# Optimization experiments

Measured on AMD Instinct MI355X. Metric: run time of the kernel, lower is better.

The kernel has to match this reference:

```python
import jax, jax.numpy as jnp
import numpy as np

# ---- static config ----
B, N, C, HF, WF = 2, 256, 256, 64, 64
PATCH = 512
ROI = 15
MARGIN = (ROI - 1) // 2
HID = 256
HEADS = 8
DEPTH = 3
FFN = 1024
NQ = 16
LN_EPS = 1e-5


def setup_inputs() -> dict:
    key = jax.random.key(0)
    ks = jax.random.split(key, 16)
    p = lambda i, shape: (0.02 * jax.random.normal(ks[i], shape, jnp.float32))
    inp = {
        "image_embeddings": jax.random.normal(ks[0], (B, C, HF, WF), jnp.float32),
        "keypoints": jax.random.uniform(ks[1], (B, N, 2), jnp.float32, 0.0, float(PATCH)),
        "keypoints_valid_mask": jax.random.randint(ks[2], (B, N), 0, 2) == 1,
        "proj_w": p(3, (HID, C)), "proj_b": jnp.zeros((HID,), jnp.float32),
        "query_embed": p(4, (NQ, HID)),
        "self_qkv_w": p(5, (DEPTH, 3 * HID, HID)), "self_qkv_b": jnp.zeros((DEPTH, 3 * HID), jnp.float32),
        "self_out_w": p(6, (DEPTH, HID, HID)), "self_out_b": jnp.zeros((DEPTH, HID), jnp.float32),
        "cross_qkv_w": p(7, (DEPTH, 3 * HID, HID)), "cross_qkv_b": jnp.zeros((DEPTH, 3 * HID), jnp.float32),
        "cross_out_w": p(8, (DEPTH, HID, HID)), "cross_out_b": jnp.zeros((DEPTH, HID), jnp.float32),
        "ffn1_w": p(9, (DEPTH, FFN, HID)), "ffn1_b": jnp.zeros((DEPTH, FFN), jnp.float32),
        "ffn2_w": p(10, (DEPTH, HID, FFN)), "ffn2_b": jnp.zeros((DEPTH, HID), jnp.float32),
        "ln1_w": jnp.ones((DEPTH, HID), jnp.float32), "ln1_b": jnp.zeros((DEPTH, HID), jnp.float32),
        "ln2_w": jnp.ones((DEPTH, HID), jnp.float32), "ln2_b": jnp.zeros((DEPTH, HID), jnp.float32),
        "ln3_w": jnp.ones((DEPTH, HID), jnp.float32), "ln3_b": jnp.zeros((DEPTH, HID), jnp.float32),
        "out_w": p(11, (4, HID)), "out_b": jnp.zeros((4,), jnp.float32),
    }
    return inp


def _layer_norm(x, w, b):
    mu = x.mean(-1, keepdims=True)
    var = ((x - mu) ** 2).mean(-1, keepdims=True)
    return (x - mu) * jax.lax.rsqrt(var + LN_EPS) * w + b


def _mha(q_in, kv_in, Wqkv, bqkv, Wo, bo, pad=None):
    # PyTorch nn.MultiheadAttention math (batch_first). pad: [B, S_kv] True=masked.
    Dh = HID // HEADS
    Wq, Wk, Wv = jnp.split(Wqkv, 3, axis=0)
    bq, bk, bv = jnp.split(bqkv, 3, axis=0)
    Bsz = q_in.shape[0]
    q = (q_in @ Wq.T + bq).reshape(Bsz, -1, HEADS, Dh)
    k = (kv_in @ Wk.T + bk).reshape(Bsz, -1, HEADS, Dh)
    v = (kv_in @ Wv.T + bv).reshape(Bsz, -1, HEADS, Dh)
    s = jnp.einsum('bqhd,bkhd->bhqk', q, k) * (Dh ** -0.5)
    if pad is not None:
        s = jnp.where(pad[:, None, None, :], -jnp.inf, s)
    a = jax.nn.softmax(s, axis=-1)
    o = jnp.einsum('bhqk,bkhd->bqhd', a, v).reshape(Bsz, -1, HID)
    return o @ Wo.T + bo


def _roi_sample(img, keypoints):
    # _get_valid_grid + F.grid_sample(bilinear, align_corners=False, zeros padding)
    rc = jnp.round(keypoints)                               # [B,N,2] (r,c), round-half-even like Python round
    off = jnp.arange(-MARGIN, MARGIN + 1, dtype=img.dtype)  # [ROI]
    gy = rc[:, :, 0][..., None, None] + off[:, None]        # [B,N,ROI,ROI] rows
    gx = rc[:, :, 1][..., None, None] + off[None, :]        # [B,N,ROI,ROI] cols
    gxn = gx / (PATCH - 1) * 2.0 - 1.0
    gyn = gy / (PATCH - 1) * 2.0 - 1.0
    invalid = (gxn < -1) | (gyn < -1) | (gxn > 1) | (gyn > 1)  # [B,N,ROI,ROI]
    gxn = jnp.where(invalid, 0.0, gxn)
    gyn = jnp.where(invalid, 0.0, gyn)
    # unnormalize onto the feature map (align_corners=False)
    x = ((gxn + 1.0) * WF - 1.0) * 0.5
    y = ((gyn + 1.0) * HF - 1.0) * 0.5
    x = x.reshape(B, -1)  # [B, P], P = N*ROI*ROI
    y = y.reshape(B, -1)
    x0f = jnp.floor(x); y0f = jnp.floor(y)
    wx = x - x0f; wy = y - y0f
    x0 = x0f.astype(jnp.int32); y0 = y0f.astype(jnp.int32)
    bidx = jnp.arange(B)[:, None]

    def tap(yi, xi, w):
        ok = (yi >= 0) & (yi < HF) & (xi >= 0) & (xi < WF)
        yc = jnp.clip(yi, 0, HF - 1)
        xc = jnp.clip(xi, 0, WF - 1)
        v = img[bidx, :, yc, xc]                 # [B,P,C] gather
        return v * (w * ok)[..., None]

    out = (tap(y0, x0, (1 - wy) * (1 - wx)) + tap(y0, x0 + 1, (1 - wy) * wx)
           + tap(y0 + 1, x0, wy * (1 - wx)) + tap(y0 + 1, x0 + 1, wy * wx))
    feat = out.reshape(B, N, ROI * ROI, C)
    feat = jnp.where(invalid.reshape(B, N, ROI * ROI)[..., None], 0.0, feat)
    return feat  # [B, N, HW, C]


def reference(image_embeddings, keypoints, keypoints_valid_mask, proj_w, proj_b,
              query_embed, self_qkv_w, self_qkv_b, self_out_w, self_out_b,
              cross_qkv_w, cross_qkv_b, cross_out_w, cross_out_b,
              ffn1_w, ffn1_b, ffn2_w, ffn2_b,
              ln1_w, ln1_b, ln2_w, ln2_b, ln3_w, ln3_b, out_w, out_b):
    feat = _roi_sample(image_embeddings, keypoints)                 # [B,N,HW,C]
    mem = jnp.einsum('bnpc,oc->bnpo', feat, proj_w) + proj_b        # 1x1 conv proj
    mem = mem.reshape(B * N, ROI * ROI, HID)
    pad = jnp.broadcast_to(~keypoints_valid_mask.reshape(-1, 1), (B * N, ROI * ROI))
    pad = pad.at[:, 0].set(False)                                    # token 0 always attendable
    tgt = jnp.broadcast_to(query_embed[None], (B * N, NQ, HID))
    for l in range(DEPTH):  # post-norm TransformerDecoderLayer, relu, eval (no dropout)
        sa = _mha(tgt, tgt, self_qkv_w[l], self_qkv_b[l], self_out_w[l], self_out_b[l])
        tgt = _layer_norm(tgt + sa, ln1_w[l], ln1_b[l])
        ca = _mha(tgt, mem, cross_qkv_w[l], cross_qkv_b[l], cross_out_w[l], cross_out_b[l], pad)
        tgt = _layer_norm(tgt + ca, ln2_w[l], ln2_b[l])
        ff = jax.nn.relu(tgt @ ffn1_w[l].T + ffn1_b[l]) @ ffn2_w[l].T + ffn2_b[l]
        tgt = _layer_norm(tgt + ff, ln3_w[l], ln3_b[l])
    out = tgt @ out_w.T + out_b                                      # [B*N, NQ, 4]
    return out.reshape(B, N, NQ, 4)
```

## Files before the change

kernel.cpp:

```cpp
#include <hip/hip_runtime.h>
#include <hip/hip_fp16.h>

#define LB __launch_bounds__(256)

typedef unsigned short u16;
typedef unsigned int   u32;
typedef __attribute__((ext_vector_type(8))) short bf16x8;
typedef __attribute__((ext_vector_type(4))) float f32x4;
typedef __attribute__((ext_vector_type(8))) u16  u16x8;

__device__ __forceinline__ u16 f2b(float f) {
    u32 u = __float_as_uint(f);
    u32 r = (u + 0x7fffu + ((u >> 16) & 1u)) >> 16;
    return (u16)r;
}
__device__ __forceinline__ float b2f(u16 h) {
    return __uint_as_float((u32)h << 16);
}

#define QSCALE 0.17677669529663687f


__global__ void k_prep(const unsigned char* __restrict__ m, int* __restrict__ valid,
                       const float* __restrict__ pb,
                       const float* __restrict__ cqkv_w,
                       const float* __restrict__ cqkv_b,
                       float* __restrict__ ckv)
{
    if (blockIdx.x == 0) {
        __shared__ int flag;
        if (threadIdx.x == 0) flag = 0;
        __syncthreads();
        int loc = 0;
        for (int off = threadIdx.x; off < 512; off += 256)
            if ((off & 3) != 0 && m[off] != 0) loc = 1;
        if (loc) atomicOr(&flag, 1);
        __syncthreads();
        const bool bytelay = (flag != 0);
        for (int s = threadIdx.x; s < 512; s += 256)
            valid[s] = bytelay ? (int)(m[s] != 0) : (int)(((const int*)m)[s] != 0);
    } else {
        const int l = blockIdx.x - 1;
        const float* Wk = cqkv_w + (size_t)l * 196608 + 65536;
        const float* Wv = cqkv_w + (size_t)l * 196608 + 131072;
        const float* kb = cqkv_b + (size_t)l * 768 + 256;
        const float* vb = cqkv_b + (size_t)l * 768 + 512;
        const int o = threadIdx.x;
        float a = 0.f, c = 0.f;
        for (int cc = 0; cc < 256; cc += 4) {
            const float4 p4 = *(const float4*)(pb + cc);
            const float4 k4 = *(const float4*)(Wk + (size_t)o * 256 + cc);
            const float4 v4 = *(const float4*)(Wv + (size_t)o * 256 + cc);
            a += p4.x * k4.x + p4.y * k4.y + p4.z * k4.z + p4.w * k4.w;
            c += p4.x * v4.x + p4.y * v4.y + p4.z * v4.z + p4.w * v4.w;
        }
        ckv[l * 512 + o]       = a + kb[o];
        ckv[l * 512 + 256 + o] = c + vb[o];
    }
}

__global__ LB void k_wconv(const float* __restrict__ s0, const float* __restrict__ s1,
                           const float* __restrict__ s2, const float* __restrict__ s3,
                           const float* __restrict__ s4, const float* __restrict__ s5,
                           const float* __restrict__ s6, u16* __restrict__ dst)
{
    const int e = blockIdx.x * 256 + threadIdx.x;
    if (e >= 3670016) return;
    float v;
    int i = e;
    if (i < 65536) v = s0[i];
    else if ((i -= 65536) < 589824) v = s1[i];
    else if ((i -= 589824) < 196608) v = s2[i];
    else if ((i -= 196608) < 589824) v = s3[i];
    else if ((i -= 589824) < 196608) v = s4[i];
    else if ((i -= 196608) < 786432) v = s5[i];
    else if ((i -= 786432) < 786432) v = s6[i];
    else if ((i -= 786432) < 393216) {
        const int l = i / 131072;
        const int r = (i - l * 131072) >> 8;
        const int c = i & 255;
        v = s3[(size_t)l * 196608 + (size_t)(256 + r) * 256 + c];
    } else {
        i -= 393216;
        v = s0[(i & 255) * 256 + (i >> 8)];
    }
    dst[e] = f2b(v);
}

__global__ LB void k_transpose(const float* __restrict__ img, u16* __restrict__ imgTb)
{
    __shared__ float tile[64][65];
    const int b  = blockIdx.z;
    const int c0 = blockIdx.y * 64;
    const int p0 = blockIdx.x * 64;
    const int t  = threadIdx.x;
    const int tr = t >> 6, tc = t & 63;
#pragma unroll
    for (int p = 0; p < 16; ++p) {
        const int i = p * 4 + tr;
        tile[i][tc] = img[((size_t)(b * 256 + c0 + i)) * 4096 + p0 + tc];
    }
    __syncthreads();
#pragma unroll
    for (int p = 0; p < 16; ++p) {
        const int jj = p * 4 + tr;
        imgTb[((size_t)(b * 4096 + p0 + jj)) * 256 + c0 + tc] = f2b(tile[tc][jj]);
    }
}

template<int BM>
__global__ LB void gemm_mfma(const u16* __restrict__ A, const u16* __restrict__ W,
                             const float* __restrict__ bias,
                             float* __restrict__ Cf, u16* __restrict__ Cb,
                             int M, int N, int K, int relu)
{
    constexpr int BN = 128;
    __shared__ u16 lds[2][(BM + BN) * 64];
    const int t = threadIdx.x;
    const int wid = t >> 6, lane = t & 63;
    const int bm = blockIdx.y * BM, bn = blockIdx.x * BN;
    const int KT = K >> 6;

    auto stage = [&](int buf, int kt) {
        const int k0 = kt * 64;
        const int rr = t >> 3;
        const int u  = t & 7;
#pragma unroll
        for (int q = 0; q < BM / 32; ++q) {
            const int r = q * 32 + rr;
            const u16* src = A + (size_t)(bm + r) * K + k0 + ((u ^ (r & 7)) << 3);
            __builtin_amdgcn_global_load_lds(
                (const __attribute__((address_space(1))) void*)src,
                (__attribute__((address_space(3))) void*)&lds[buf][q * 2048 + wid * 512],
                16, 0, 0);
        }
#pragma unroll
        for (int q = 0; q < 4; ++q) {
            const int r = q * 32 + rr;
            const u16* src = W + (size_t)(bn + r) * K + k0 + ((u ^ (r & 7)) << 3);
            __builtin_amdgcn_global_load_lds(
                (const __attribute__((address_space(1))) void*)src,
                (__attribute__((address_space(3))) void*)&lds[buf][BM * 64 + q * 2048 + wid * 512],
                16, 0, 0);
        }
    };

    const int wr = wid >> 1, wc = wid & 1;
    constexpr int MR = BM / 32;
    f32x4 acc[MR][4];
    const f32x4 z = {0.f, 0.f, 0.f, 0.f};
#pragma unroll
    for (int mi = 0; mi < MR; ++mi)
#pragma unroll
        for (int ni = 0; ni < 4; ++ni) acc[mi][ni] = z;

    const int r16 = lane & 15, kg = lane >> 4;

    stage(0, 0);
    int cur = 0;
    for (int kt = 0; kt < KT; ++kt) {
        asm volatile("s_waitcnt vmcnt(0)" ::: "memory");
        __syncthreads();
        if (kt + 1 < KT) stage(cur ^ 1, kt + 1);
        const u16* pA = lds[cur];
        const u16* pB = lds[cur] + BM * 64;
#pragma unroll
        for (int kk = 0; kk < 2; ++kk) {
            const int s = kk * 4 + kg;
            bf16x8 afr[MR], bfr[4];
#pragma unroll
            for (int mi = 0; mi < MR; ++mi) {
                const int r = wr * (BM / 2) + mi * 16 + r16;
                afr[mi] = *(const bf16x8*)(pA + r * 64 + ((s ^ (r & 7)) << 3));
            }
#pragma unroll
            for (int ni = 0; ni < 4; ++ni) {
                const int c = wc * 64 + ni * 16 + r16;
                bfr[ni] = *(const bf16x8*)(pB + c * 64 + ((s ^ (c & 7)) << 3));
            }
#pragma unroll
            for (int mi = 0; mi < MR; ++mi)
#pragma unroll
                for (int ni = 0; ni < 4; ++ni)
                    acc[mi][ni] = __builtin_amdgcn_mfma_f32_16x16x32_bf16(
                        afr[mi], bfr[ni], acc[mi][ni], 0, 0, 0);
        }
        cur ^= 1;
    }

#pragma unroll
    for (int mi = 0; mi < MR; ++mi) {
#pragma unroll
        for (int ni = 0; ni < 4; ++ni) {
            const int col = bn + wc * 64 + ni * 16 + r16;
            const float bs = bias ? bias[col] : 0.0f;
#pragma unroll
            for (int rg = 0; rg < 4; ++rg) {
                const int row = bm + wr * (BM / 2) + mi * 16 + kg * 4 + rg;
                float v = acc[mi][ni][rg] + bs;
                if (relu) v = fmaxf(v, 0.0f);
                if (Cf) Cf[(size_t)row * N + col] = v;
                if (Cb) Cb[(size_t)row * N + col] = f2b(v);
            }
        }
    }
}

__global__ LB void gemm_ln(const u16* __restrict__ A, const u16* __restrict__ W,
                           const float* __restrict__ bias,
                           float* __restrict__ tgt, u16* __restrict__ tgtb,
                           const float* __restrict__ lnw, const float* __restrict__ lnb,
                           int K,
                           const float* __restrict__ ow, const float* __restrict__ ob,
                           float* __restrict__ outp)
{
    __shared__ u16 lA[32 * 64];
    __shared__ u16 lB[256 * 64];
    __shared__ float psum[2][32];
    __shared__ float psq[2][32];
    __shared__ float hsum[2][32][4];
    const int t = threadIdx.x;
    const int wid = t >> 6, lane = t & 63;
    const int r16 = lane & 15, kg = lane >> 4;
    const int wr = wid >> 1, wc = wid & 1;
    const int bm = blockIdx.x * 32;
    const int KT = K >> 6;

    f32x4 acc[8];
    const f32x4 z = {0.f, 0.f, 0.f, 0.f};
#pragma unroll
    for (int ni = 0; ni < 8; ++ni) acc[ni] = z;

    for (int kt = 0; kt < KT; ++kt) {
        const int k0 = kt * 64;
        const int rr = t >> 3;
        const int u  = t & 7;
        {
            const int r = rr;
            const u16* src = A + (size_t)(bm + r) * K + k0 + ((u ^ (r & 7)) << 3);
            __builtin_amdgcn_global_load_lds(
                (const __attribute__((address_space(1))) void*)src,
                (__attribute__((address_space(3))) void*)&lA[wid * 512],
                16, 0, 0);
        }
#pragma unroll
        for (int q = 0; q < 8; ++q) {
            const int r = q * 32 + rr;
            const u16* src = W + (size_t)r * K + k0 + ((u ^ (r & 7)) << 3);
            __builtin_amdgcn_global_load_lds(
                (const __attribute__((address_space(1))) void*)src,
                (__attribute__((address_space(3))) void*)&lB[q * 2048 + wid * 512],
                16, 0, 0);
        }
        asm volatile("s_waitcnt vmcnt(0)" ::: "memory");
        __syncthreads();
#pragma unroll
        for (int kk = 0; kk < 2; ++kk) {
            const int s = kk * 4 + kg;
            const int ra = wr * 16 + r16;
            const bf16x8 afr = *(const bf16x8*)(lA + ra * 64 + ((s ^ (ra & 7)) << 3));
#pragma unroll
            for (int ni = 0; ni < 8; ++ni) {
                const int c = wc * 128 + ni * 16 + r16;
                const bf16x8 bfr = *(const bf16x8*)(lB + c * 64 + ((s ^ (c & 7)) << 3));
                acc[ni] = __builtin_amdgcn_mfma_f32_16x16x32_bf16(afr, bfr, acc[ni], 0, 0, 0);
            }
        }
        __syncthreads();
    }

    float xv[4][8];
    float bcol[8], wcol[8], bncol[8];
#pragma unroll
    for (int ni = 0; ni < 8; ++ni) {
        const int c = wc * 128 + ni * 16 + r16;
        bcol[ni]  = bias[c];
        wcol[ni]  = lnw[c];
        bncol[ni] = lnb[c];
    }
#pragma unroll
    for (int rg = 0; rg < 4; ++rg) {
        const int row = bm + wr * 16 + kg * 4 + rg;
#pragma unroll
        for (int ni = 0; ni < 8; ++ni) {
            const int c = wc * 128 + ni * 16 + r16;
            xv[rg][ni] = tgt[(size_t)row * 256 + c] + acc[ni][rg] + bcol[ni];
        }
    }
#pragma unroll
    for (int rg = 0; rg < 4; ++rg) {
        float s = 0.f;
#pragma unroll
        for (int ni = 0; ni < 8; ++ni) s += xv[rg][ni];
#pragma unroll
        for (int m = 1; m < 16; m <<= 1) s += __shfl_xor(s, m);
        if (r16 == 0) psum[wc][wr * 16 + kg * 4 + rg] = s;
    }
    __syncthreads();
    float mu[4];
#pragma unroll
    for (int rg = 0; rg < 4; ++rg) {
        const int rl = wr * 16 + kg * 4 + rg;
        mu[rg] = (psum[0][rl] + psum[1][rl]) * (1.0f / 256.0f);
    }
#pragma unroll
    for (int rg = 0; rg < 4; ++rg) {
        float q = 0.f;
#pragma unroll
        for (int ni = 0; ni < 8; ++ni) {
            const float d = xv[rg][ni] - mu[rg];
            q += d * d;
        }
#pragma unroll
        for (int m = 1; m < 16; m <<= 1) q += __shfl_xor(q, m);
        if (r16 == 0) psq[wc][wr * 16 + kg * 4 + rg] = q;
    }
    __syncthreads();
    float onorm[4][8];
#pragma unroll
    for (int rg = 0; rg < 4; ++rg) {
        const int rl = wr * 16 + kg * 4 + rg;
        const int row = bm + rl;
        const float var = (psq[0][rl] + psq[1][rl]) * (1.0f / 256.0f);
        const float inv = 1.0f / sqrtf(var + 1e-5f);
#pragma unroll
        for (int ni = 0; ni < 8; ++ni) {
            const int c = wc * 128 + ni * 16 + r16;
            const float o = (xv[rg][ni] - mu[rg]) * inv * wcol[ni] + bncol[ni];
            onorm[rg][ni] = o;
            tgt[(size_t)row * 256 + c]  = o;
            tgtb[(size_t)row * 256 + c] = f2b(o);
        }
    }

    if (outp) {
#pragma unroll
        for (int j = 0; j < 4; ++j) {
            float wj[8];
#pragma unroll
            for (int ni = 0; ni < 8; ++ni)
                wj[ni] = ow[j * 256 + wc * 128 + ni * 16 + r16];
#pragma unroll
            for (int rg = 0; rg < 4; ++rg) {
                float p = 0.f;
#pragma unroll
                for (int ni = 0; ni < 8; ++ni) p += onorm[rg][ni] * wj[ni];
#pragma unroll
                for (int m = 1; m < 16; m <<= 1) p += __shfl_xor(p, m);
                if (r16 == 0) hsum[wc][wr * 16 + kg * 4 + rg][j] = p;
            }
        }
        __syncthreads();
        if (t < 128) {
            const int row = t >> 2, j = t & 3;
            outp[(size_t)(bm + row) * 4 + j] =
                hsum[0][row][j] + hsum[1][row][j] + ob[j];
        }
    }
}

__global__ LB void k_init_tgt(float* __restrict__ tgt, u16* __restrict__ tgtb,
                              const float* __restrict__ qe)
{
    const int e = blockIdx.x * 256 + threadIdx.x;
    const int c = e & 255;
    const int row = e >> 8;
    const int i = row & 15;
    const float v = qe[(i << 8) | c];
    tgt[e] = v;
    tgtb[e] = f2b(v);
}

__global__ LB void k_self_attn(const u16* __restrict__ QKV, u16* __restrict__ O)
{
    __shared__ __align__(16) u16 arena[4][1536];
    const int t = threadIdx.x;
    const int lane = t & 63, wid = t >> 6;
    const int r16 = lane & 15, kg = lane >> 4;
    const int blk = blockIdx.x;
    const int s = blk >> 1;
    const int h = (blk & 1) * 4 + wid;

    u16* p_lds = &arena[wid][0];
    u16* vT    = &arena[wid][512];

    const bf16x8 qfr = *(const bf16x8*)(QKV + (size_t)(s * 16 + r16) * 768 + h * 32 + kg * 8);
    const bf16x8 kfr = *(const bf16x8*)(QKV + (size_t)(s * 16 + r16) * 768 + 256 + h * 32 + kg * 8);
    f32x4 sv = {0.f, 0.f, 0.f, 0.f};
    sv = __builtin_amdgcn_mfma_f32_16x16x32_bf16(qfr, kfr, sv, 0, 0, 0);

    float ev[4], rowsum[4];
#pragma unroll
    for (int rg = 0; rg < 4; ++rg) ev[rg] = sv[rg] * QSCALE;
#pragma unroll
    for (int rg = 0; rg < 4; ++rg) {
        float mx = ev[rg];
#pragma unroll
        for (int m = 1; m < 16; m <<= 1) mx = fmaxf(mx, __shfl_xor(mx, m));
        ev[rg] = __expf(ev[rg] - mx);
        float ps = ev[rg];
#pragma unroll
        for (int m = 1; m < 16; m <<= 1) ps += __shfl_xor(ps, m);
        rowsum[rg] = ps;
    }

#pragma unroll
    for (int rg = 0; rg < 4; ++rg)
        p_lds[(kg * 4 + rg) * 32 + r16] = f2b(ev[rg]);
    {
        const int zq = lane & 15, zc = 16 + (lane >> 4) * 4;
#pragma unroll
        for (int j = 0; j < 4; ++j) p_lds[zq * 32 + zc + j] = 0;
    }
    {
        const int key = lane >> 2, ch8 = (lane & 3) * 8;
        const u16x8 v = *(const u16x8*)(QKV + (size_t)(s * 16 + key) * 768 + 512 + h * 32 + ch8);
#pragma unroll
        for (int j = 0; j < 8; ++j)
            vT[(ch8 + j) * 32 + key] = ((const u16*)&v)[j];
        const int zc0 = lane >> 1, zk0 = 16 + (lane & 1) * 8;
#pragma unroll
        for (int j = 0; j < 8; ++j) vT[zc0 * 32 + zk0 + j] = 0;
    }

#pragma unroll
    for (int ct = 0; ct < 2; ++ct) {
        const bf16x8 pa = *(const bf16x8*)(p_lds + r16 * 32 + kg * 8);
        const bf16x8 vb = *(const bf16x8*)(vT + (ct * 16 + r16) * 32 + kg * 8);
        f32x4 ao = {0.f, 0.f, 0.f, 0.f};
        ao = __builtin_amdgcn_mfma_f32_16x16x32_bf16(pa, vb, ao, 0, 0, 0);
#pragma unroll
        for (int rg = 0; rg < 4; ++rg) {
            const int q = kg * 4 + rg;
            O[(size_t)(s * 16 + q) * 256 + h * 32 + ct * 16 + r16] = f2b(ao[rg] / rowsum[rg]);
        }
    }
}

__global__ LB void k_cross_attn(const u16* __restrict__ Qb,
                                const u16* __restrict__ KV, int kvs,
                                const float* __restrict__ ckv,
                                const int* __restrict__ valid,
                                const float* __restrict__ kps,
                                u16* __restrict__ O)
{
    __shared__ __align__(16) char arena[64832];
    u16* Wm  = (u16*)arena;
    u16* WmT = (u16*)(arena + 14400);

    const int t = threadIdx.x;
    const int lane = t & 63, wid = t >> 6;
    const int r16 = lane & 15, kg = lane >> 4;
    const int blk = blockIdx.x;
    const int s = blk >> 1;
    const int h = (blk & 1) * 4 + wid;
    const int b = s >> 8, n = s & 255;

    u16* buf = (u16*)(arena + 22848 + wid * 10496);
    u16* p_b = (u16*)(arena + 22848 + wid * 10496 + 2048);
    u16* QP  = p_b;

    for (int e = t; e < 16208; e += 256) ((u32*)arena)[e] = 0;
    __syncthreads();

    const float kpy = kps[(b * 256 + n) * 2 + 0];
    const float kpx = kps[(b * 256 + n) * 2 + 1];
    const float gx0 = rintf(kpx) - 7.0f;
    const float gy0 = rintf(kpy) - 7.0f;
    const float gxn0 = gx0 / 511.0f * 2.0f - 1.0f;
    const float gyn0 = gy0 / 511.0f * 2.0f - 1.0f;
    const float xb = ((gxn0 + 1.f) * 64.f - 1.f) * 0.5f;
    const float yb = ((gyn0 + 1.f) * 64.f - 1.f) * 0.5f;
    const int x0b = (int)floorf(xb);
    const int y0b = (int)floorf(yb);

    if (t < 225) {
        const int iy = t / 15, ix = t - iy * 15;
        const float gy = rintf(kpy) + (float)(iy - 7);
        const float gx = rintf(kpx) + (float)(ix - 7);
        const float gxn = gx / 511.0f * 2.0f - 1.0f;
        const float gyn = gy / 511.0f * 2.0f - 1.0f;
        const bool inval = (gxn < -1.f) || (gyn < -1.f) || (gxn > 1.f) || (gyn > 1.f);
        const float x = ((gxn + 1.f) * 64.f - 1.f) * 0.5f;
        const float y = ((gyn + 1.f) * 64.f - 1.f) * 0.5f;
        const float x0f = floorf(x), y0f = floorf(y);
        const float wx = x - x0f, wy = y - y0f;
        const int x0 = (int)x0f, y0 = (int)y0f;
#pragma unroll
        for (int tt = 0; tt < 4; ++tt) {
            const int dy = tt >> 1, dx = tt & 1;
            const int yi = y0 + dy, xi = x0 + dx;
            const bool ok = (yi >= 0) && (yi < 64) && (xi >= 0) && (xi < 64) && !inval;
            const float w = (dy ? wy : 1.f - wy) * (dx ? wx : 1.f - wx);
            if (ok) {
                const int cell = (yi - y0b) * 4 + (xi - x0b);
                const u16 wb = f2b(w);
                Wm[t * 32 + ((((cell >> 3) ^ (t & 3)) << 3) | (cell & 7))] = wb;
                WmT[cell * 264 + t] = wb;
            }
        }
    }
    const int cell = lane >> 2, ch8 = (lane & 3) * 8;
    const int cy = cell >> 2, cx = cell & 3;
    const int py = min(max(y0b + cy, 0), 63);
    const int px = min(max(x0b + cx, 0), 63);
    const size_t texidx = (size_t)(b * 4096 + py * 64 + px) * kvs + h * 32 + ch8;
    *(u16x8*)(buf + cell * 32 + ch8) = *(const u16x8*)(KV + texidx);
    const bool vld = valid[s] != 0;
    __syncthreads();

    {
        const bf16x8 qfr = *(const bf16x8*)(Qb + (size_t)(s * 16 + r16) * 256 + h * 32 + kg * 8);
        const bf16x8 tfr = *(const bf16x8*)(buf + r16 * 32 + kg * 8);
        f32x4 aq = {0.f, 0.f, 0.f, 0.f};
        aq = __builtin_amdgcn_mfma_f32_16x16x32_bf16(qfr, tfr, aq, 0, 0, 0);
#pragma unroll
        for (int rg = 0; rg < 4; ++rg)
            QP[(kg * 4 + rg) * 40 + r16] = f2b(aq[rg]);
    }

    float ev[4][15];
    {
        const bf16x8 afr = *(const bf16x8*)(QP + r16 * 40 + kg * 8);
#pragma unroll
        for (int tile = 0; tile < 15; ++tile) {
            const int p = tile * 16 + r16;
            const int rc = p < 225 ? p : 224;
            const bf16x8 bfr = *(const bf16x8*)(Wm + rc * 32 + ((kg ^ (rc & 3)) << 3));
            f32x4 acc = {0.f, 0.f, 0.f, 0.f};
            acc = __builtin_amdgcn_mfma_f32_16x16x32_bf16(afr, bfr, acc, 0, 0, 0);
#pragma unroll
            for (int rg = 0; rg < 4; ++rg) {
                float sv = acc[rg] * QSCALE;
                if (p > 224) sv = -1e30f;
                if (!vld && p > 0) sv = -1e30f;
                ev[rg][tile] = sv;
            }
        }
    }
    float rowsumv[4];
#pragma unroll
    for (int rg = 0; rg < 4; ++rg) {
        float mx = -1e30f;
#pragma unroll
        for (int k = 0; k < 15; ++k) mx = fmaxf(mx, ev[rg][k]);
#pragma unroll
        for (int m = 1; m < 16; m <<= 1) mx = fmaxf(mx, __shfl_xor(mx, m));
        float ps = 0.f;
#pragma unroll
        for (int k = 0; k < 15; ++k) {
            ev[rg][k] = __expf(ev[rg][k] - mx);
            ps += ev[rg][k];
        }
#pragma unroll
        for (int m = 1; m < 16; m <<= 1) ps += __shfl_xor(ps, m);
        rowsumv[rg] = ps;
    }

#pragma unroll
    for (int rg = 0; rg < 4; ++rg)
#pragma unroll
        for (int k = 0; k < 15; ++k) {
            const int p = k * 16 + r16;
            if (p < 225) p_b[(kg * 4 + rg) * 264 + p] = f2b(ev[rg][k]);
        }
    for (int e = lane; e < 496; e += 64) {
        const int row = e / 31;
        p_b[row * 264 + 225 + (e - row * 31)] = 0;
    }

    {
        const u16x8 v = *(const u16x8*)(KV + texidx + 256);
#pragma unroll
        for (int j = 0; j < 8; ++j)
            buf[(ch8 + j) * 32 + cell] = ((const u16*)&v)[j];
        const int zr = lane & 15, zc0 = 16 + (lane >> 4) * 4;
#pragma unroll
        for (int j = 0; j < 4; ++j) buf[zr * 32 + zc0 + j] = 0;
    }

    f32x4 pw = {0.f, 0.f, 0.f, 0.f};
#pragma unroll
    for (int ks = 0; ks < 8; ++ks) {
        const bf16x8 pa = *(const bf16x8*)(p_b + r16 * 264 + ks * 32 + kg * 8);
        const bf16x8 wb = *(const bf16x8*)(WmT + r16 * 264 + ks * 32 + kg * 8);
        pw = __builtin_amdgcn_mfma_f32_16x16x32_bf16(pa, wb, pw, 0, 0, 0);
    }

#pragma unroll
    for (int rg = 0; rg < 4; ++rg)
        QP[(kg * 4 + rg) * 40 + r16] = f2b(pw[rg]);
    {
        const int zq = lane & 15, zc0 = 16 + (lane >> 4) * 4;
#pragma unroll
        for (int j = 0; j < 4; ++j) QP[zq * 40 + zc0 + j] = 0;
    }

#pragma unroll
    for (int ct = 0; ct < 2; ++ct) {
        const bf16x8 pa = *(const bf16x8*)(QP + r16 * 40 + kg * 8);
        const bf16x8 vb = *(const bf16x8*)(buf + (ct * 16 + r16) * 32 + kg * 8);
        f32x4 ao = {0.f, 0.f, 0.f, 0.f};
        ao = __builtin_amdgcn_mfma_f32_16x16x32_bf16(pa, vb, ao, 0, 0, 0);
#pragma unroll
        for (int rg = 0; rg < 4; ++rg) {
            const int q = kg * 4 + rg;
            const int ch = h * 32 + ct * 16 + r16;
            const float val = ao[rg] / rowsumv[rg] + ckv[256 + ch];
            O[(size_t)(s * 16 + q) * 256 + ch] = f2b(val);
        }
    }
}

extern "C" void kernel_launch(void* const* d_in, const int* in_sizes, int n_in,
                              void* d_out, int out_size, void* d_ws, size_t ws_size,
                              hipStream_t stream)
{
    const float* img          = (const float*)d_in[0];
    const float* kps          = (const float*)d_in[1];
    const unsigned char* vmsk = (const unsigned char*)d_in[2];
    const float* proj_w       = (const float*)d_in[3];
    const float* proj_b       = (const float*)d_in[4];
    const float* query_embed  = (const float*)d_in[5];
    const float* self_qkv_w   = (const float*)d_in[6];
    const float* self_qkv_b   = (const float*)d_in[7];
    const float* self_out_w   = (const float*)d_in[8];
    const float* self_out_b   = (const float*)d_in[9];
    const float* cross_qkv_w  = (const float*)d_in[10];
    const float* cross_qkv_b  = (const float*)d_in[11];
    const float* cross_out_w  = (const float*)d_in[12];
    const float* cross_out_b  = (const float*)d_in[13];
    const float* ffn1_w       = (const float*)d_in[14];
    const float* ffn1_b       = (const float*)d_in[15];
    const float* ffn2_w       = (const float*)d_in[16];
    const float* ffn2_b       = (const float*)d_in[17];
    const float* ln1_w        = (const float*)d_in[18];
    const float* ln1_b        = (const float*)d_in[19];
    const float* ln2_w        = (const float*)d_in[20];
    const float* ln2_b        = (const float*)d_in[21];
    const float* ln3_w        = (const float*)d_in[22];
    const float* ln3_b        = (const float*)d_in[23];
    const float* out_w        = (const float*)d_in[24];
    const float* out_b        = (const float*)d_in[25];
    float* out = (float*)d_out;

    char* W8 = (char*)d_ws;
    size_t off = 0;
    auto alloc = [&](size_t bytes) { void* p = W8 + off; off += (bytes + 255) & ~(size_t)255; return p; };
    float* tgt   = (float*)alloc(2097152 * 4);
    u16* Qb      = (u16*)alloc(2097152 * 2);
    u16* Sb16    = (u16*)alloc(6291456 * 2);
    float* ckv   = (float*)alloc(3 * 512 * 4);
    u16* imgTb   = (u16*)alloc(2097152 * 2);
    u16* KVb3    = (u16*)alloc(12582912 * 2);
    u16* tgtb    = (u16*)alloc(2097152 * 2);
    u16* Abuf    = (u16*)alloc(2097152 * 2);
    u16* Hbuf    = (u16*)alloc(8388608 * 2);
    u16* wAll    = (u16*)alloc(3670016 * 2);
    u16* WcombB  = (u16*)alloc(393216 * 2);
    int* valid   = (int*)alloc(512 * 4);

    u16* wProj  = wAll;
    u16* wSQKV  = wProj + 65536;
    u16* wSOut  = wSQKV + 589824;
    u16* wCQKV  = wSOut + 196608;
    u16* wCOut  = wCQKV + 589824;
    u16* wF1    = wCOut + 196608;
    u16* wF2    = wF1 + 786432;
    u16* wCKV3  = wF2 + 786432;
    u16* wProjT = wCKV3 + 393216;

    k_prep<<<4, 256, 0, stream>>>(vmsk, valid, proj_b, cross_qkv_w, cross_qkv_b, ckv);
    k_wconv<<<14336, 256, 0, stream>>>(proj_w, self_qkv_w, self_out_w, cross_qkv_w,
                                       cross_out_w, ffn1_w, ffn2_w, wAll);
    k_transpose<<<dim3(64, 4, 2), 256, 0, stream>>>(img, imgTb);
    gemm_mfma<64><<<dim3(2, 24), 256, 0, stream>>>(wCKV3, wProjT, nullptr,
                                                   nullptr, WcombB, 1536, 256, 256, 0);
    gemm_mfma<128><<<dim3(12, 64), 256, 0, stream>>>(imgTb, WcombB, nullptr,
                                                     nullptr, KVb3, 8192, 1536, 256, 0);
    k_init_tgt<<<8192, 256, 0, stream>>>(tgt, tgtb, query_embed);

    for (int l = 0; l < 3; ++l) {
        const int last = (l == 2);
        gemm_mfma<64><<<dim3(6, 128), 256, 0, stream>>>(tgtb, wSQKV + (size_t)l * 196608,
            self_qkv_b + (size_t)l * 768, nullptr, Sb16, 8192, 768, 256, 0);
        k_self_attn<<<1024, 256, 0, stream>>>(Sb16, Abuf);
        gemm_ln<<<256, 256, 0, stream>>>(Abuf, wSOut + (size_t)l * 65536,
            self_out_b + (size_t)l * 256, tgt, tgtb,
            ln1_w + (size_t)l * 256, ln1_b + (size_t)l * 256, 256,
            nullptr, nullptr, nullptr);

        gemm_mfma<64><<<dim3(2, 128), 256, 0, stream>>>(tgtb, wCQKV + (size_t)l * 196608,
            cross_qkv_b + (size_t)l * 768, nullptr, Qb, 8192, 256, 256, 0);
        k_cross_attn<<<1024, 256, 0, stream>>>(Qb, KVb3 + (size_t)l * 512, 1536,
                                               ckv + (size_t)l * 512, valid, kps, Abuf);
        gemm_ln<<<256, 256, 0, stream>>>(Abuf, wCOut + (size_t)l * 65536,
            cross_out_b + (size_t)l * 256, tgt, tgtb,
            ln2_w + (size_t)l * 256, ln2_b + (size_t)l * 256, 256,
            nullptr, nullptr, nullptr);

        gemm_mfma<64><<<dim3(8, 128), 256, 0, stream>>>(tgtb, wF1 + (size_t)l * 262144,
            ffn1_b + (size_t)l * 1024, nullptr, Hbuf, 8192, 1024, 256, 1);
        gemm_ln<<<256, 256, 0, stream>>>(Hbuf, wF2 + (size_t)l * 262144,
            ffn2_b + (size_t)l * 256, tgt, tgtb,
            ln3_w + (size_t)l * 256, ln3_b + (size_t)l * 256, 1024,
            last ? out_w : nullptr, last ? out_b : nullptr, last ? out : nullptr);
    }
}
```

Baseline: 378.3 us.

## Fuse cross-attention Q projection into attention kernel and merge prep into weight conversion

The per-layer Q projection GEMM for cross-attention is removed; each attention block now computes its head's Q slice from tgtb and the bf16 Q weights with MFMA and stores it into shared memory, adding the Q bias from the ckv buffer. The k_prep kernel is folded into k_wconv as extra blocks. The K-bias precomputation is replaced by storing the raw Q bias, since the K-side constant shifts every score in a row equally and so cancels in softmax. This saves three launches and the Qb round trip through global memory. In exchange each block repeats the tgt row loads, and the two blocks per sample each read 8 K-steps of weights.

```diff
diff --git a/kernel.cpp b/kernel.cpp
--- a/kernel.cpp
+++ b/kernel.cpp
@@ -21,49 +21,45 @@
 #define QSCALE 0.17677669529663687f
 
 
-__global__ void k_prep(const unsigned char* __restrict__ m, int* __restrict__ valid,
-                       const float* __restrict__ pb,
-                       const float* __restrict__ cqkv_w,
-                       const float* __restrict__ cqkv_b,
-                       float* __restrict__ ckv)
-{
-    if (blockIdx.x == 0) {
-        __shared__ int flag;
-        if (threadIdx.x == 0) flag = 0;
-        __syncthreads();
-        int loc = 0;
-        for (int off = threadIdx.x; off < 512; off += 256)
-            if ((off & 3) != 0 && m[off] != 0) loc = 1;
-        if (loc) atomicOr(&flag, 1);
-        __syncthreads();
-        const bool bytelay = (flag != 0);
-        for (int s = threadIdx.x; s < 512; s += 256)
-            valid[s] = bytelay ? (int)(m[s] != 0) : (int)(((const int*)m)[s] != 0);
-    } else {
-        const int l = blockIdx.x - 1;
-        const float* Wk = cqkv_w + (size_t)l * 196608 + 65536;
-        const float* Wv = cqkv_w + (size_t)l * 196608 + 131072;
-        const float* kb = cqkv_b + (size_t)l * 768 + 256;
-        const float* vb = cqkv_b + (size_t)l * 768 + 512;
-        const int o = threadIdx.x;
-        float a = 0.f, c = 0.f;
-        for (int cc = 0; cc < 256; cc += 4) {
-            const float4 p4 = *(const float4*)(pb + cc);
-            const float4 k4 = *(const float4*)(Wk + (size_t)o * 256 + cc);
-            const float4 v4 = *(const float4*)(Wv + (size_t)o * 256 + cc);
-            a += p4.x * k4.x + p4.y * k4.y + p4.z * k4.z + p4.w * k4.w;
-            c += p4.x * v4.x + p4.y * v4.y + p4.z * v4.z + p4.w * v4.w;
-        }
-        ckv[l * 512 + o]       = a + kb[o];
-        ckv[l * 512 + 256 + o] = c + vb[o];
-    }
-}
-
 __global__ LB void k_wconv(const float* __restrict__ s0, const float* __restrict__ s1,
                            const float* __restrict__ s2, const float* __restrict__ s3,
                            const float* __restrict__ s4, const float* __restrict__ s5,
-                           const float* __restrict__ s6, u16* __restrict__ dst)
+                           const float* __restrict__ s6, u16* __restrict__ dst,
+                           const unsigned char* __restrict__ m, int* __restrict__ valid,
+                           const float* __restrict__ pb,
+                           const float* __restrict__ cqkv_b,
+                           float* __restrict__ ckv)
 {
+    if (blockIdx.x >= 14336) {
+        const int pblk = blockIdx.x - 14336;
+        if (pblk == 0) {
+            __shared__ int flag;
+            if (threadIdx.x == 0) flag = 0;
+            __syncthreads();
+            int loc = 0;
+            for (int off = threadIdx.x; off < 512; off += 256)
+                if ((off & 3) != 0 && m[off] != 0) loc = 1;
+            if (loc) atomicOr(&flag, 1);
+            __syncthreads();
+            const bool bytelay = (flag != 0);
+            for (int s = threadIdx.x; s < 512; s += 256)
+                valid[s] = bytelay ? (int)(m[s] != 0) : (int)(((const int*)m)[s] != 0);
+        } else {
+            const int l = pblk - 1;
+            const float* Wv = s3 + (size_t)l * 196608 + 131072;
+            const float* vb = cqkv_b + (size_t)l * 768 + 512;
+            const int o = threadIdx.x;
+            float c = 0.f;
+            for (int cc = 0; cc < 256; cc += 4) {
+                const float4 p4 = *(const float4*)(pb + cc);
+                const float4 v4 = *(const float4*)(Wv + (size_t)o * 256 + cc);
+                c += p4.x * v4.x + p4.y * v4.y + p4.z * v4.z + p4.w * v4.w;
+            }
+            ckv[l * 512 + o]       = cqkv_b[(size_t)l * 768 + o];
+            ckv[l * 512 + 256 + o] = c + vb[o];
+        }
+        return;
+    }
     const int e = blockIdx.x * 256 + threadIdx.x;
     if (e >= 3670016) return;
     float v;
@@ -437,7 +433,8 @@
     }
 }
 
-__global__ LB void k_cross_attn(const u16* __restrict__ Qb,
+__global__ LB void k_cross_attn(const u16* __restrict__ tgtb,
+                                const u16* __restrict__ wQ,
                                 const u16* __restrict__ KV, int kvs,
                                 const float* __restrict__ ckv,
                                 const int* __restrict__ valid,
@@ -500,6 +497,20 @@
             }
         }
     }
+#pragma unroll
+    for (int ct = 0; ct < 2; ++ct) {
+        f32x4 aq = {0.f, 0.f, 0.f, 0.f};
+#pragma unroll
+        for (int ks = 0; ks < 8; ++ks) {
+            const bf16x8 ta = *(const bf16x8*)(tgtb + (size_t)(s * 16 + r16) * 256 + ks * 32 + kg * 8);
+            const bf16x8 wb = *(const bf16x8*)(wQ + (size_t)(h * 32 + ct * 16 + r16) * 256 + ks * 32 + kg * 8);
+            aq = __builtin_amdgcn_mfma_f32_16x16x32_bf16(ta, wb, aq, 0, 0, 0);
+        }
+        const float bq = ckv[h * 32 + ct * 16 + r16];
+#pragma unroll
+        for (int rg = 0; rg < 4; ++rg)
+            QP[(kg * 4 + rg) * 40 + ct * 16 + r16] = f2b(aq[rg] + bq);
+    }
     const int cell = lane >> 2, ch8 = (lane & 3) * 8;
     const int cy = cell >> 2, cx = cell & 3;
     const int py = min(max(y0b + cy, 0), 63);
@@ -510,7 +521,7 @@
     __syncthreads();
 
     {
-        const bf16x8 qfr = *(const bf16x8*)(Qb + (size_t)(s * 16 + r16) * 256 + h * 32 + kg * 8);
+        const bf16x8 qfr = *(const bf16x8*)(QP + r16 * 40 + kg * 8);
         const bf16x8 tfr = *(const bf16x8*)(buf + r16 * 32 + kg * 8);
         f32x4 aq = {0.f, 0.f, 0.f, 0.f};
         aq = __builtin_amdgcn_mfma_f32_16x16x32_bf16(qfr, tfr, aq, 0, 0, 0);
@@ -648,7 +659,6 @@
     size_t off = 0;
     auto alloc = [&](size_t bytes) { void* p = W8 + off; off += (bytes + 255) & ~(size_t)255; return p; };
     float* tgt   = (float*)alloc(2097152 * 4);
-    u16* Qb      = (u16*)alloc(2097152 * 2);
     u16* Sb16    = (u16*)alloc(6291456 * 2);
     float* ckv   = (float*)alloc(3 * 512 * 4);
     u16* imgTb   = (u16*)alloc(2097152 * 2);
@@ -670,9 +680,9 @@
     u16* wCKV3  = wF2 + 786432;
     u16* wProjT = wCKV3 + 393216;
 
-    k_prep<<<4, 256, 0, stream>>>(vmsk, valid, proj_b, cross_qkv_w, cross_qkv_b, ckv);
-    k_wconv<<<14336, 256, 0, stream>>>(proj_w, self_qkv_w, self_out_w, cross_qkv_w,
-                                       cross_out_w, ffn1_w, ffn2_w, wAll);
+    k_wconv<<<14340, 256, 0, stream>>>(proj_w, self_qkv_w, self_out_w, cross_qkv_w,
+                                       cross_out_w, ffn1_w, ffn2_w, wAll,
+                                       vmsk, valid, proj_b, cross_qkv_b, ckv);
     k_transpose<<<dim3(64, 4, 2), 256, 0, stream>>>(img, imgTb);
     gemm_mfma<64><<<dim3(2, 24), 256, 0, stream>>>(wCKV3, wProjT, nullptr,
                                                    nullptr, WcombB, 1536, 256, 256, 0);
@@ -690,9 +700,8 @@
             ln1_w + (size_t)l * 256, ln1_b + (size_t)l * 256, 256,
             nullptr, nullptr, nullptr);
 
-        gemm_mfma<64><<<dim3(2, 128), 256, 0, stream>>>(tgtb, wCQKV + (size_t)l * 196608,
-            cross_qkv_b + (size_t)l * 768, nullptr, Qb, 8192, 256, 256, 0);
-        k_cross_attn<<<1024, 256, 0, stream>>>(Qb, KVb3 + (size_t)l * 512, 1536,
+        k_cross_attn<<<1024, 256, 0, stream>>>(tgtb, wCQKV + (size_t)l * 196608,
+                                               KVb3 + (size_t)l * 512, 1536,
                                                ckv + (size_t)l * 512, valid, kps, Abuf);
         gemm_ln<<<256, 256, 0, stream>>>(Abuf, wCOut + (size_t)l * 65536,
             cross_out_b + (size_t)l * 256, tgt, tgtb,
```

Result: no change. 371.0 us (-1.9%).
